# Performance work log

Measured on AMD Instinct MI355X. Metric: run time of the kernel, lower is better.

Reference implementation:

```python
import jax, jax.numpy as jnp
import numpy as np

N_NODES = 50000
N_EDGES = 1600000
D = 128        # fea_dim == hidden_units == dim_z
L = 3          # num_layers


def _gin_params(key, scale=0.05):
    ks = jax.random.split(key, 7)
    return dict(
        W1=jax.random.normal(ks[0], (L, D, D), jnp.float32) * scale,
        b1=jnp.zeros((L, D), jnp.float32),
        W2=jax.random.normal(ks[1], (L, D, D), jnp.float32) * scale,
        b2=jnp.zeros((L, D), jnp.float32),
        eps=jnp.zeros((L,), jnp.float32),
        Wout=jax.random.normal(ks[2], (D, D), jnp.float32) * scale,
        bout=jnp.zeros((D,), jnp.float32),
    )


def setup_inputs() -> dict:
    key = jax.random.key(0)
    k_x, k_s, k_d, k_m, k_sd = jax.random.split(key, 5)
    inp = {
        'x': jax.random.normal(k_x, (N_NODES, D), jnp.float32),
        'edge_src': jax.random.randint(k_s, (N_EDGES,), 0, N_NODES, jnp.int32),
        'edge_dst': jax.random.randint(k_d, (N_EDGES,), 0, N_NODES, jnp.int32),
    }
    for pref, k in (('mean_', k_m), ('std_', k_sd)):
        for name, v in _gin_params(k).items():
            inp[pref + name] = v
    inp['ln_gamma'] = jnp.ones((D,), jnp.float32)
    inp['ln_beta'] = jnp.zeros((D,), jnp.float32)
    return inp


def _gin(x, src, dst, W1, b1, W2, b2, eps, Wout, bout):
    # Standard GIN: h = MLP((1+eps)*h + sum_{j->i} h_j), Sigmoid activation
    h = x
    n = x.shape[0]
    for l in range(L):
        agg = jax.ops.segment_sum(h[src], dst, num_segments=n)  # [N, D]
        h = (1.0 + eps[l]) * h + agg
        h = jax.nn.sigmoid(h @ W1[l] + b1[l]) @ W2[l] + b2[l]
    return h @ Wout + bout  # [N, dim_z]


def _layernorm(v, g, b, eps=1e-5):
    m = jnp.mean(v, axis=-1, keepdims=True)
    var = jnp.var(v, axis=-1, keepdims=True)
    return (v - m) * jax.lax.rsqrt(var + eps) * g + b


def reference(x, edge_src, edge_dst,
              mean_W1, mean_b1, mean_W2, mean_b2, mean_eps, mean_Wout, mean_bout,
              std_W1, std_b1, std_W2, std_b2, std_eps, std_Wout, std_bout,
              ln_gamma, ln_beta):
    mean_v = _layernorm(_gin(x, edge_src, edge_dst, mean_W1, mean_b1, mean_W2,
                             mean_b2, mean_eps, mean_Wout, mean_bout),
                        ln_gamma, ln_beta)
    # NOTE: source applies bn_mean to the std path too (faithful to bug)
    std_v = _layernorm(_gin(x, edge_src, edge_dst, std_W1, std_b1, std_W2,
                            std_b2, std_eps, std_Wout, std_bout),
                       ln_gamma, ln_beta)
    epsilon = jax.random.normal(jax.random.key(42), mean_v.shape, mean_v.dtype)
    samples = mean_v + epsilon * std_v
    return (samples, mean_v, std_v)
```

## Files before the change

kernel.cpp:

```cpp
#include <hip/hip_runtime.h>
#include <math.h>

#define NNODES 50000
#define NEDGES 1600000
#define DIM    128
#define NHID   (NNODES * DIM)
#define TPB    256
#define NTILES ((NNODES + 63) / 64)

#define NBINS  196
#define BINSZ  256
#define EPT    16
#define CHUNK  (TPB * EPT)
#define NCHUNKS ((NEDGES + CHUNK - 1) / CHUNK)
#define BINCAP 10240

#define WMAT   (128 * 136)
#define NWMAT  14

typedef unsigned short bf16_t;
typedef __attribute__((ext_vector_type(8))) short short8;
typedef __attribute__((ext_vector_type(4))) float f32x4;
typedef __attribute__((ext_vector_type(2))) float f32x2;

__device__ __forceinline__ float bf_lo(unsigned u) { return __uint_as_float(u << 16); }
__device__ __forceinline__ float bf_hi(unsigned u) { return __uint_as_float(u & 0xFFFF0000u); }
__device__ __forceinline__ bf16_t f2bf(float f) {
    unsigned u = __float_as_uint(f);
    u += 0x7FFFu + ((u >> 16) & 1u);
    return (bf16_t)(u >> 16);
}
__device__ __forceinline__ unsigned pack2bf(float a, float b) {
    return (unsigned)f2bf(a) | ((unsigned)f2bf(b) << 16);
}

union S8U { short8 v; uint4 u4; unsigned us[4]; };

__global__ __launch_bounds__(TPB) void bin_hist_kernel(
    const int* __restrict__ dst, int* __restrict__ gcnt)
{
    __shared__ int lcnt[NBINS];
    const int tid = threadIdx.x;
    for (int i = tid; i < NBINS; i += TPB) lcnt[i] = 0;
    __syncthreads();
    const int base = blockIdx.x * CHUNK;
    #pragma unroll
    for (int k = 0; k < EPT; ++k) {
        int e = base + k * TPB + tid;
        if (e < NEDGES) atomicAdd(&lcnt[dst[e] >> 8], 1);
    }
    __syncthreads();
    for (int i = tid; i < NBINS; i += TPB) {
        int c = lcnt[i];
        if (c) atomicAdd(&gcnt[i], c);
    }
}

__global__ __launch_bounds__(64) void bin_scan_kernel(
    const int* __restrict__ gcnt, int* __restrict__ start, int* __restrict__ bcur,
    int* __restrict__ off)
{
    const int lane = threadIdx.x;
    int c[4];
    int s = 0;
    #pragma unroll
    for (int k = 0; k < 4; ++k) {
        int b = 4 * lane + k;
        c[k] = (b < NBINS) ? gcnt[b] : 0;
        s += c[k];
    }
    int incl = s;
    #pragma unroll
    for (int d = 1; d < 64; d <<= 1) {
        int t = __shfl_up(incl, d);
        if (lane >= d) incl += t;
    }
    int excl = incl - s;
    #pragma unroll
    for (int k = 0; k < 4; ++k) {
        int b = 4 * lane + k;
        if (b < NBINS) { start[b] = excl; bcur[b] = excl; }
        excl += c[k];
    }
    if (lane == 63) { start[NBINS] = excl; off[NNODES] = excl; }
}

__global__ __launch_bounds__(TPB) void bin_scatter_kernel(
    const int* __restrict__ src, const int* __restrict__ dst,
    int* __restrict__ bcur, unsigned* __restrict__ bucket)
{
    __shared__ int lcnt[NBINS];
    __shared__ int lcur[NBINS];
    const int tid = threadIdx.x;
    for (int i = tid; i < NBINS; i += TPB) lcnt[i] = 0;
    __syncthreads();

    unsigned pk[EPT];
    int bn[EPT];
    const int base = blockIdx.x * CHUNK;
    #pragma unroll
    for (int k = 0; k < EPT; ++k) {
        int e = base + k * TPB + tid;
        int b = -1; unsigned p = 0;
        if (e < NEDGES) {
            int d = dst[e];
            int s = src[e];
            b = d >> 8;
            p = ((unsigned)(d & 255) << 16) | (unsigned)s;
            atomicAdd(&lcnt[b], 1);
        }
        pk[k] = p; bn[k] = b;
    }
    __syncthreads();
    for (int i = tid; i < NBINS; i += TPB) {
        int c = lcnt[i];
        lcur[i] = (c > 0) ? atomicAdd(&bcur[i], c) : 0;
    }
    __syncthreads();
    #pragma unroll
    for (int k = 0; k < EPT; ++k) {
        if (bn[k] >= 0) {
            int p = atomicAdd(&lcur[bn[k]], 1);
            bucket[p] = pk[k];
        }
    }
}

__global__ __launch_bounds__(TPB) void build_csr_kernel(
    const int* __restrict__ start, unsigned* __restrict__ bucket,
    int* __restrict__ off)
{
    __shared__ unsigned se[BINCAP];
    __shared__ int lcnt[BINSZ];
    __shared__ int lofs[BINSZ];
    __shared__ int wsum[4];
    const int tid = threadIdx.x;
    const int b = blockIdx.x;
    const int j0 = start[b], j1 = start[b + 1];
    const int n = j1 - j0;

    lcnt[tid] = 0;
    for (int i = tid; i < n; i += TPB) se[i] = bucket[j0 + i];
    __syncthreads();
    for (int i = tid; i < n; i += TPB) atomicAdd(&lcnt[se[i] >> 16], 1);
    __syncthreads();

    const int lane = tid & 63, wid = tid >> 6;
    int v = lcnt[tid];
    int s = v;
    #pragma unroll
    for (int d = 1; d < 64; d <<= 1) {
        int t = __shfl_up(s, d);
        if (lane >= d) s += t;
    }
    if (lane == 63) wsum[wid] = s;
    __syncthreads();
    if (tid == 0) {
        int a = 0;
        #pragma unroll
        for (int k = 0; k < 4; ++k) { int t = wsum[k]; wsum[k] = a; a += t; }
    }
    __syncthreads();
    int excl = wsum[wid] + s - v;
    lofs[tid] = excl;
    int node = b * BINSZ + tid;
    if (node < NNODES) off[node] = j0 + excl;
    __syncthreads();

    for (int i = tid; i < n; i += TPB) {
        unsigned e = se[i];
        int pos = atomicAdd(&lofs[e >> 16], 1);
        bucket[j0 + pos] = e & 0xFFFFu;
    }
}

__global__ __launch_bounds__(TPB) void convert_weights_kernel(
    const float* __restrict__ W1_0, const float* __restrict__ W2_0,
    const float* __restrict__ Wo_0,
    const float* __restrict__ W1_1, const float* __restrict__ W2_1,
    const float* __restrict__ Wo_1,
    bf16_t* __restrict__ wpre)
{
    const int b = blockIdx.x;
    const int p = b / 7, s = b % 7;
    const float* W;
    if (s < 3)      W = (p ? W1_1 : W1_0) + (size_t)s * DIM * DIM;
    else if (s < 6) W = (p ? W2_1 : W2_0) + (size_t)(s - 3) * DIM * DIM;
    else            W = p ? Wo_1 : Wo_0;
    bf16_t* dst = wpre + (size_t)b * WMAT;

    for (int idx = threadIdx.x; idx < 128 * 16; idx += TPB) {
        int n = idx & 127, koct = idx >> 7;
        float f[8];
        #pragma unroll
        for (int j = 0; j < 8; ++j) f[j] = W[(8 * koct + j) * 128 + n];
        uint4 u;
        u.x = pack2bf(f[0], f[1]); u.y = pack2bf(f[2], f[3]);
        u.z = pack2bf(f[4], f[5]); u.w = pack2bf(f[6], f[7]);
        *(uint4*)&dst[n * 136 + 8 * koct] = u;
    }
}

__global__ __launch_bounds__(TPB) void gather_agg_f32_kernel(
    const float* __restrict__ h, const int* __restrict__ off,
    const unsigned* __restrict__ bucket, float* __restrict__ acat)
{
    int node = blockIdx.x * (TPB / 64) + (threadIdx.x >> 6);
    int lane = threadIdx.x & 63;
    if (node >= NNODES) return;
    int j0 = off[node], j1 = off[node + 1];
    const float* base = h + 2 * lane;
    float ax = 0.0f, ay = 0.0f;
    int j = j0;
    for (; j + 16 <= j1; j += 16) {
        unsigned s[16];
        #pragma unroll
        for (int k = 0; k < 16; ++k) s[k] = bucket[j + k];
        float2 v[16];
        #pragma unroll
        for (int k = 0; k < 16; ++k) v[k] = *(const float2*)(base + (size_t)s[k] * DIM);
        #pragma unroll
        for (int k = 0; k < 16; ++k) { ax += v[k].x; ay += v[k].y; }
    }
    for (; j + 8 <= j1; j += 8) {
        unsigned s[8];
        #pragma unroll
        for (int k = 0; k < 8; ++k) s[k] = bucket[j + k];
        float2 v[8];
        #pragma unroll
        for (int k = 0; k < 8; ++k) v[k] = *(const float2*)(base + (size_t)s[k] * DIM);
        #pragma unroll
        for (int k = 0; k < 8; ++k) { ax += v[k].x; ay += v[k].y; }
    }
    for (; j < j1; ++j) {
        float2 v0 = *(const float2*)(base + (size_t)bucket[j] * DIM);
        ax += v0.x; ay += v0.y;
    }
    f32x2 r; r.x = ax; r.y = ay;
    __builtin_nontemporal_store(r, (f32x2*)(acat + (size_t)node * 256 + 2 * lane));
}

__global__ __launch_bounds__(TPB) void gather_cat_kernel(
    const bf16_t* __restrict__ hc, const int* __restrict__ off,
    const unsigned* __restrict__ bucket, float* __restrict__ acat)
{
    int node = blockIdx.x * (TPB / 64) + (threadIdx.x >> 6);
    int lane = threadIdx.x & 63;
    if (node >= NNODES) return;
    int j0 = off[node], j1 = off[node + 1];
    const uint2* base = (const uint2*)hc + lane;
    float a0 = 0.f, a1 = 0.f, a2 = 0.f, a3 = 0.f;
    int j = j0;
    for (; j + 16 <= j1; j += 16) {
        unsigned s[16];
        #pragma unroll
        for (int k = 0; k < 16; ++k) s[k] = bucket[j + k];
        uint2 u[16];
        #pragma unroll
        for (int k = 0; k < 16; ++k) u[k] = base[(size_t)s[k] * 64];
        #pragma unroll
        for (int k = 0; k < 16; ++k) {
            a0 += bf_lo(u[k].x); a1 += bf_hi(u[k].x);
            a2 += bf_lo(u[k].y); a3 += bf_hi(u[k].y);
        }
    }
    for (; j + 8 <= j1; j += 8) {
        unsigned s[8];
        #pragma unroll
        for (int k = 0; k < 8; ++k) s[k] = bucket[j + k];
        uint2 u[8];
        #pragma unroll
        for (int k = 0; k < 8; ++k) u[k] = base[(size_t)s[k] * 64];
        #pragma unroll
        for (int k = 0; k < 8; ++k) {
            a0 += bf_lo(u[k].x); a1 += bf_hi(u[k].x);
            a2 += bf_lo(u[k].y); a3 += bf_hi(u[k].y);
        }
    }
    for (; j < j1; ++j) {
        uint2 u = base[(size_t)bucket[j] * 64];
        a0 += bf_lo(u.x); a1 += bf_hi(u.x);
        a2 += bf_lo(u.y); a3 += bf_hi(u.y);
    }
    f32x4 r; r.x = a0; r.y = a1; r.z = a2; r.w = a3;
    __builtin_nontemporal_store(r, (f32x4*)(acat + (size_t)node * 256 + 4 * lane));
}

template <class HinT, int INSTRIDE>
__global__ __launch_bounds__(TPB, 4) void fused_layer_kernel(
    const HinT* __restrict__ hin, const float* __restrict__ acat, int aggByPath,
    const float* __restrict__ eps0, const float* __restrict__ eps1, int eps_idx,
    const float* __restrict__ W1_0, const float* __restrict__ b1_0,
    const float* __restrict__ W2_0, const float* __restrict__ b2_0,
    const float* __restrict__ W1_1, const float* __restrict__ b1_1,
    const float* __restrict__ W2_1, const float* __restrict__ b2_1,
    const bf16_t* __restrict__ wpre,
    bf16_t* __restrict__ out)
{
    __shared__ short sWt[128 * 136];
    __shared__ short y1b[64 * 136];

    const int p = (blockIdx.x >= NTILES) ? 1 : 0;
    const int t = blockIdx.x - p * NTILES;
    const int l = eps_idx;
    const float* W1 = p ? W1_1 : W1_0;
    const float* b1 = p ? b1_1 : b1_0;
    const float* W2 = p ? W2_1 : W2_0;
    const float* b2 = p ? b2_1 : b2_0;
    const float* epsp = p ? eps1 : eps0;
    const HinT* hbase = (INSTRIDE == 256) ? (hin + p * 128) : hin;
    const float* abase = acat + (aggByPath ? p * 128 : 0);
    bf16_t* ob = out + p * 128;

    const int tid = threadIdx.x;
    if (wpre) {
        const uint4* s = (const uint4*)(wpre + (size_t)(p * 7 + l) * WMAT);
        uint4* d = (uint4*)sWt;
        #pragma unroll
        for (int i = 0; i < 9; ++i) {
            int idx = i * 256 + tid;
            if (idx < WMAT / 8) d[idx] = s[idx];
        }
    } else {
        #pragma unroll
        for (int it = 0; it < 8; ++it) {
            int idx = it * 256 + tid;
            int n = idx & 127, koct = idx >> 7;
            float f1[8];
            #pragma unroll
            for (int j = 0; j < 8; ++j) f1[j] = W1[(8 * koct + j) * 128 + n];
            uint4 u1;
            u1.x = pack2bf(f1[0], f1[1]); u1.y = pack2bf(f1[2], f1[3]);
            u1.z = pack2bf(f1[4], f1[5]); u1.w = pack2bf(f1[6], f1[7]);
            *(uint4*)&sWt[n * 136 + 8 * koct] = u1;
        }
    }
    __syncthreads();

    const int lane = tid & 63, w = tid >> 6;
    const int m = lane & 15, quad = lane >> 4;

    const float scale = 1.0f + epsp[eps_idx];
    float b1v[8], b2v[8];
    #pragma unroll
    for (int c = 0; c < 8; ++c) { b1v[c] = b1[16 * c + m]; b2v[c] = b2[16 * c + m]; }

    const int arow = min(t * 64 + 16 * w + m, NNODES - 1);

    short8 afh[4], afl[4];
    #pragma unroll
    for (int k0 = 0; k0 < 4; ++k0) {
        const int kb = 32 * k0 + 8 * quad;
        float zf[8];
        if constexpr (sizeof(HinT) == 4) {
            const float* hp = (const float*)hbase + (size_t)arow * INSTRIDE + kb;
            float4 h0 = *(const float4*)hp;
            float4 h1 = *(const float4*)(hp + 4);
            zf[0] = h0.x; zf[1] = h0.y; zf[2] = h0.z; zf[3] = h0.w;
            zf[4] = h1.x; zf[5] = h1.y; zf[6] = h1.z; zf[7] = h1.w;
        } else {
            uint4 hu = *(const uint4*)((const bf16_t*)hbase + (size_t)arow * INSTRIDE + kb);
            zf[0] = bf_lo(hu.x); zf[1] = bf_hi(hu.x);
            zf[2] = bf_lo(hu.y); zf[3] = bf_hi(hu.y);
            zf[4] = bf_lo(hu.z); zf[5] = bf_hi(hu.z);
            zf[6] = bf_lo(hu.w); zf[7] = bf_hi(hu.w);
        }
        const float* ap = abase + (size_t)arow * 256 + kb;
        float4 a0 = *(const float4*)ap;
        float4 a1 = *(const float4*)(ap + 4);
        zf[0] = fmaf(scale, zf[0], a0.x); zf[1] = fmaf(scale, zf[1], a0.y);
        zf[2] = fmaf(scale, zf[2], a0.z); zf[3] = fmaf(scale, zf[3], a0.w);
        zf[4] = fmaf(scale, zf[4], a1.x); zf[5] = fmaf(scale, zf[5], a1.y);
        zf[6] = fmaf(scale, zf[6], a1.z); zf[7] = fmaf(scale, zf[7], a1.w);
        S8U hi;
        hi.us[0] = pack2bf(zf[0], zf[1]); hi.us[1] = pack2bf(zf[2], zf[3]);
        hi.us[2] = pack2bf(zf[4], zf[5]); hi.us[3] = pack2bf(zf[6], zf[7]);
        afh[k0] = hi.v;
        S8U lo;
        float lw[8];
        lw[0] = zf[0] - bf_lo(hi.us[0]); lw[1] = zf[1] - bf_hi(hi.us[0]);
        lw[2] = zf[2] - bf_lo(hi.us[1]); lw[3] = zf[3] - bf_hi(hi.us[1]);
        lw[4] = zf[4] - bf_lo(hi.us[2]); lw[5] = zf[5] - bf_hi(hi.us[2]);
        lw[6] = zf[6] - bf_lo(hi.us[3]); lw[7] = zf[7] - bf_hi(hi.us[3]);
        lo.us[0] = pack2bf(lw[0], lw[1]); lo.us[1] = pack2bf(lw[2], lw[3]);
        lo.us[2] = pack2bf(lw[4], lw[5]); lo.us[3] = pack2bf(lw[6], lw[7]);
        afl[k0] = lo.v;
    }

    f32x4 acc[8];
    #pragma unroll
    for (int c = 0; c < 8; ++c) acc[c] = (f32x4){0.f, 0.f, 0.f, 0.f};
    #pragma unroll
    for (int k0 = 0; k0 < 4; ++k0) {
        const int kb = 32 * k0 + 8 * quad;
        #pragma unroll
        for (int c = 0; c < 8; ++c) {
            short8 bfr = *(const short8*)&sWt[(16 * c + m) * 136 + kb];
            acc[c] = __builtin_amdgcn_mfma_f32_16x16x32_bf16(afl[k0], bfr, acc[c], 0, 0, 0);
            acc[c] = __builtin_amdgcn_mfma_f32_16x16x32_bf16(afh[k0], bfr, acc[c], 0, 0, 0);
        }
    }

    const int rloc0 = 16 * w + 4 * quad;
    #pragma unroll
    for (int r = 0; r < 4; ++r) {
        #pragma unroll
        for (int c = 0; c < 8; ++c) {
            float y = acc[c][r] + b1v[c];
            y = 1.0f / (1.0f + expf(-y));
            y1b[(rloc0 + r) * 136 + 16 * c + m] = (short)f2bf(y);
        }
    }
    __syncthreads();

    if (wpre) {
        const uint4* s = (const uint4*)(wpre + (size_t)(p * 7 + 3 + l) * WMAT);
        uint4* d = (uint4*)sWt;
        #pragma unroll
        for (int i = 0; i < 9; ++i) {
            int idx = i * 256 + tid;
            if (idx < WMAT / 8) d[idx] = s[idx];
        }
    } else {
        #pragma unroll
        for (int it = 0; it < 8; ++it) {
            int idx = it * 256 + tid;
            int n = idx & 127, koct = idx >> 7;
            float f2[8];
            #pragma unroll
            for (int j = 0; j < 8; ++j) f2[j] = W2[(8 * koct + j) * 128 + n];
            uint4 u2;
            u2.x = pack2bf(f2[0], f2[1]); u2.y = pack2bf(f2[2], f2[3]);
            u2.z = pack2bf(f2[4], f2[5]); u2.w = pack2bf(f2[6], f2[7]);
            *(uint4*)&sWt[n * 136 + 8 * koct] = u2;
        }
    }
    __syncthreads();

    f32x4 acc2[8];
    #pragma unroll
    for (int c = 0; c < 8; ++c) acc2[c] = (f32x4){0.f, 0.f, 0.f, 0.f};
    #pragma unroll
    for (int k0 = 0; k0 < 4; ++k0) {
        const int kb = 32 * k0 + 8 * quad;
        short8 a2 = *(const short8*)&y1b[(16 * w + m) * 136 + kb];
        #pragma unroll
        for (int c = 0; c < 8; ++c) {
            short8 b2f = *(const short8*)&sWt[(16 * c + m) * 136 + kb];
            acc2[c] = __builtin_amdgcn_mfma_f32_16x16x32_bf16(a2, b2f, acc2[c], 0, 0, 0);
        }
    }

    const int row0 = t * 64 + 16 * w + 4 * quad;
    #pragma unroll
    for (int r = 0; r < 4; ++r) {
        const int grow = row0 + r;
        if (grow < NNODES) {
            bf16_t* op = ob + (size_t)grow * 256 + m;
            #pragma unroll
            for (int c = 0; c < 8; ++c) op[16 * c] = f2bf(acc2[c][r] + b2v[c]);
        }
    }
}

__global__ __launch_bounds__(TPB) void final_proj_kernel(
    const bf16_t* __restrict__ hc,
    const float* __restrict__ Wo0, const float* __restrict__ bo0,
    const float* __restrict__ Wo1, const float* __restrict__ bo1,
    const float* __restrict__ gamma, const float* __restrict__ beta,
    const bf16_t* __restrict__ wpre,
    float* __restrict__ M, float* __restrict__ V)
{
    __shared__ short sWt[128 * 136];

    const int p = (blockIdx.x >= NTILES) ? 1 : 0;
    const int t = blockIdx.x - p * NTILES;
    const float* W = p ? Wo1 : Wo0;
    const float* bias = p ? bo1 : bo0;
    const bf16_t* hbase = hc + p * 128;
    float* out = p ? V : M;

    const int tid = threadIdx.x;
    if (wpre) {
        const uint4* s = (const uint4*)(wpre + (size_t)(p * 7 + 6) * WMAT);
        uint4* d = (uint4*)sWt;
        #pragma unroll
        for (int i = 0; i < 9; ++i) {
            int idx = i * 256 + tid;
            if (idx < WMAT / 8) d[idx] = s[idx];
        }
    } else {
        #pragma unroll
        for (int it = 0; it < 8; ++it) {
            int idx = it * 256 + tid;
            int n = idx & 127, koct = idx >> 7;
            float f[8];
            #pragma unroll
            for (int j = 0; j < 8; ++j) f[j] = W[(8 * koct + j) * 128 + n];
            uint4 u;
            u.x = pack2bf(f[0], f[1]); u.y = pack2bf(f[2], f[3]);
            u.z = pack2bf(f[4], f[5]); u.w = pack2bf(f[6], f[7]);
            *(uint4*)&sWt[n * 136 + 8 * koct] = u;
        }
    }
    __syncthreads();

    const int lane = tid & 63, w = tid >> 6;
    const int m = lane & 15, quad = lane >> 4;

    short8 bf[32];
    #pragma unroll
    for (int c = 0; c < 8; ++c)
        #pragma unroll
        for (int k0 = 0; k0 < 4; ++k0)
            bf[c * 4 + k0] = *(const short8*)&sWt[(16 * c + m) * 136 + 32 * k0 + 8 * quad];

    float bias_v[8], g_v[8], bt_v[8];
    #pragma unroll
    for (int c = 0; c < 8; ++c) {
        bias_v[c] = bias[16 * c + m];
        g_v[c] = gamma[16 * c + m];
        bt_v[c] = beta[16 * c + m];
    }

    const int arow = min(t * 64 + 16 * w + m, NNODES - 1);
    short8 af[4];
    #pragma unroll
    for (int k0 = 0; k0 < 4; ++k0)
        af[k0] = *(const short8*)(hbase + (size_t)arow * 256 + 32 * k0 + 8 * quad);

    f32x4 acc[8];
    #pragma unroll
    for (int c = 0; c < 8; ++c) acc[c] = (f32x4){0.f, 0.f, 0.f, 0.f};
    #pragma unroll
    for (int k0 = 0; k0 < 4; ++k0)
        #pragma unroll
        for (int c = 0; c < 8; ++c)
            acc[c] = __builtin_amdgcn_mfma_f32_16x16x32_bf16(
                af[k0], bf[c * 4 + k0], acc[c], 0, 0, 0);

    const int row0 = t * 64 + 16 * w + 4 * quad;
    #pragma unroll
    for (int r = 0; r < 4; ++r) {
        const int grow = row0 + r;
        float y[8];
        #pragma unroll
        for (int c = 0; c < 8; ++c) y[c] = acc[c][r] + bias_v[c];
        float s1 = 0.f, s2 = 0.f;
        #pragma unroll
        for (int c = 0; c < 8; ++c) { s1 += y[c]; s2 = fmaf(y[c], y[c], s2); }
        #pragma unroll
        for (int d = 1; d < 16; d <<= 1) {
            s1 += __shfl_xor(s1, d);
            s2 += __shfl_xor(s2, d);
        }
        float mean = s1 * (1.0f / DIM);
        float var  = s2 * (1.0f / DIM) - mean * mean;
        float rstd = rsqrtf(var + 1e-5f);
        if (grow < NNODES) {
            float* op = out + (size_t)grow * DIM + m;
            #pragma unroll
            for (int c = 0; c < 8; ++c)
                op[16 * c] = fmaf((y[c] - mean) * rstd, g_v[c], bt_v[c]);
        }
    }
}

__device__ __forceinline__ unsigned rotl32(unsigned x, int r) {
    return (x << r) | (x >> (32 - r));
}

__device__ __forceinline__ unsigned threefry_xor(unsigned c0, unsigned c1) {
    const unsigned k0 = 0u, k1 = 42u;
    const unsigned k2 = k0 ^ k1 ^ 0x1BD11BDAu;
    unsigned x0 = c0 + k0;
    unsigned x1 = c1 + k1;
#define TF_ROUND(R) { x0 += x1; x1 = rotl32(x1, R); x1 ^= x0; }
    TF_ROUND(13) TF_ROUND(15) TF_ROUND(26) TF_ROUND(6)
    x0 += k1; x1 += k2 + 1u;
    TF_ROUND(17) TF_ROUND(29) TF_ROUND(16) TF_ROUND(24)
    x0 += k2; x1 += k0 + 2u;
    TF_ROUND(13) TF_ROUND(15) TF_ROUND(26) TF_ROUND(6)
    x0 += k0; x1 += k1 + 3u;
    TF_ROUND(17) TF_ROUND(29) TF_ROUND(16) TF_ROUND(24)
    x0 += k1; x1 += k2 + 4u;
    TF_ROUND(13) TF_ROUND(15) TF_ROUND(26) TF_ROUND(6)
    x0 += k2; x1 += k0 + 5u;
#undef TF_ROUND
    return x0 ^ x1;
}

__device__ __forceinline__ float bits_to_normal(unsigned bits) {
    float f = __uint_as_float((bits >> 9) | 0x3F800000u) - 1.0f;
    const float lo = -0.99999994f;
    float u = __fadd_rn(__fmul_rn(f, 2.0f), lo);
    u = fmaxf(lo, u);
    float w = -log1pf(-(u * u));
    float p;
    if (w < 5.0f) {
        w -= 2.5f;
        p = 2.81022636e-08f;
        p = fmaf(p, w, 3.43273939e-07f);
        p = fmaf(p, w, -3.5233877e-06f);
        p = fmaf(p, w, -4.39150654e-06f);
        p = fmaf(p, w, 0.00021858087f);
        p = fmaf(p, w, -0.00125372503f);
        p = fmaf(p, w, -0.00417768164f);
        p = fmaf(p, w, 0.246640727f);
        p = fmaf(p, w, 1.50140941f);
    } else {
        w = sqrtf(w) - 3.0f;
        p = -0.000200214257f;
        p = fmaf(p, w, 0.000100950558f);
        p = fmaf(p, w, 0.00134934322f);
        p = fmaf(p, w, -0.00367342844f);
        p = fmaf(p, w, 0.00573950773f);
        p = fmaf(p, w, -0.0076224613f);
        p = fmaf(p, w, 0.00943887047f);
        p = fmaf(p, w, 1.00167406f);
        p = fmaf(p, w, 2.83297682f);
    }
    return 1.41421356f * (p * u);
}

__global__ __launch_bounds__(TPB) void samples_kernel(
    const float* __restrict__ mean_v, const float* __restrict__ std_v,
    float* __restrict__ samples)
{
    int t = blockIdx.x * TPB + threadIdx.x;
    if (t >= NHID / 4) return;
    float4 m = ((const float4*)mean_v)[t];
    float4 s = ((const float4*)std_v)[t];
    float e[4];
    #pragma unroll
    for (int q = 0; q < 4; q++) {
        unsigned i = 4u * (unsigned)t + (unsigned)q;
        e[q] = bits_to_normal(threefry_xor(0u, i));
    }
    f32x4 r;
    r.x = fmaf(e[0], s.x, m.x);
    r.y = fmaf(e[1], s.y, m.y);
    r.z = fmaf(e[2], s.z, m.z);
    r.w = fmaf(e[3], s.w, m.w);
    __builtin_nontemporal_store(r, (f32x4*)samples + t);
}

extern "C" void kernel_launch(void* const* d_in, const int* in_sizes, int n_in,
                              void* d_out, int out_size, void* d_ws, size_t ws_size,
                              hipStream_t stream)
{
    const float* x     = (const float*)d_in[0];
    const int*   esrc  = (const int*)d_in[1];
    const int*   edst  = (const int*)d_in[2];
    const float* prm[2][7];
    for (int p = 0; p < 2; p++)
        for (int i = 0; i < 7; i++)
            prm[p][i] = (const float*)d_in[3 + p * 7 + i];
    const float* gamma = (const float*)d_in[17];
    const float* beta  = (const float*)d_in[18];

    float*  S  = (float*)d_out;
    float*  M  = S + NHID;
    float*  V  = M + NHID;
    bf16_t* Hc = (bf16_t*)S;
    float*  ACAT = M;

    int* gcnt  = (int*)d_ws;
    int* start = gcnt + NBINS;
    int* bcur  = start + NBINS + 1;
    int* off   = bcur + NBINS;
    unsigned* bucket = (unsigned*)(off + NNODES + 1);

    size_t csr_bytes = ((char*)(bucket + NEDGES)) - (char*)d_ws;
    size_t wpre_off  = (csr_bytes + 15) & ~(size_t)15;
    size_t need      = wpre_off + (size_t)NWMAT * WMAT * sizeof(bf16_t);
    bf16_t* wpre = (ws_size >= need) ? (bf16_t*)((char*)d_ws + wpre_off) : nullptr;

    const dim3 gChunk(NCHUNKS);
    const dim3 gBin(NBINS);
    const dim3 gGather((NNODES + (TPB / 64) - 1) / (TPB / 64));
    const dim3 gTile2(2 * NTILES);
    const dim3 gSamp((NHID / 4 + TPB - 1) / TPB);

    hipMemsetAsync(gcnt, 0, NBINS * sizeof(int), stream);
    if (wpre)
        convert_weights_kernel<<<dim3(NWMAT), TPB, 0, stream>>>(
            prm[0][0], prm[0][2], prm[0][5], prm[1][0], prm[1][2], prm[1][5], wpre);
    bin_hist_kernel<<<gChunk, TPB, 0, stream>>>(edst, gcnt);
    bin_scan_kernel<<<1, 64, 0, stream>>>(gcnt, start, bcur, off);
    bin_scatter_kernel<<<gChunk, TPB, 0, stream>>>(esrc, edst, bcur, bucket);
    build_csr_kernel<<<gBin, TPB, 0, stream>>>(start, bucket, off);

    gather_agg_f32_kernel<<<gGather, TPB, 0, stream>>>(x, off, bucket, ACAT);

    fused_layer_kernel<float, DIM><<<gTile2, TPB, 0, stream>>>(
        x, ACAT, 0, prm[0][4], prm[1][4], 0,
        prm[0][0], prm[0][1], prm[0][2], prm[0][3],
        prm[1][0], prm[1][1], prm[1][2], prm[1][3], wpre, Hc);

    for (int l = 1; l < 3; l++) {
        gather_cat_kernel<<<gGather, TPB, 0, stream>>>(Hc, off, bucket, ACAT);
        fused_layer_kernel<bf16_t, 256><<<gTile2, TPB, 0, stream>>>(
            Hc, ACAT, 1, prm[0][4], prm[1][4], l,
            prm[0][0] + (size_t)l * DIM * DIM, prm[0][1] + l * DIM,
            prm[0][2] + (size_t)l * DIM * DIM, prm[0][3] + l * DIM,
            prm[1][0] + (size_t)l * DIM * DIM, prm[1][1] + l * DIM,
            prm[1][2] + (size_t)l * DIM * DIM, prm[1][3] + l * DIM, wpre, Hc);
    }

    final_proj_kernel<<<gTile2, TPB, 0, stream>>>(
        Hc, prm[0][5], prm[0][6], prm[1][5], prm[1][6], gamma, beta, wpre, M, V);

    samples_kernel<<<gSamp, TPB, 0, stream>>>(M, V, S);
}
```

Before: 640.1 us.

## Drop histogram pass via fixed-capacity bins; prefetch tile inputs before weight staging

The CSR build no longer runs a separate histogram kernel and memset. Edges are scattered straight into fixed-capacity per-bin slots held in the output buffer, and the scan runs afterwards on the final bin cursors. This removes one full read pass over the destination array and two launches, but it assumes no bin exceeds BINCAP edges. The fused layer and output kernels also issue their activation loads before the weight-staging barrier, and the output kernel reads B fragments from LDS inside the MFMA loop instead of holding 32 of them in registers; the layer kernel's launch bounds drop from 4 to 3 blocks per SM.

```diff
diff --git a/kernel.cpp b/kernel.cpp
--- a/kernel.cpp
+++ b/kernel.cpp
@@ -36,58 +36,15 @@
 
 union S8U { short8 v; uint4 u4; unsigned us[4]; };
 
-__global__ __launch_bounds__(TPB) void bin_hist_kernel(
-    const int* __restrict__ dst, int* __restrict__ gcnt)
-{
-    __shared__ int lcnt[NBINS];
-    const int tid = threadIdx.x;
-    for (int i = tid; i < NBINS; i += TPB) lcnt[i] = 0;
-    __syncthreads();
-    const int base = blockIdx.x * CHUNK;
-    #pragma unroll
-    for (int k = 0; k < EPT; ++k) {
-        int e = base + k * TPB + tid;
-        if (e < NEDGES) atomicAdd(&lcnt[dst[e] >> 8], 1);
-    }
-    __syncthreads();
-    for (int i = tid; i < NBINS; i += TPB) {
-        int c = lcnt[i];
-        if (c) atomicAdd(&gcnt[i], c);
-    }
-}
-
-__global__ __launch_bounds__(64) void bin_scan_kernel(
-    const int* __restrict__ gcnt, int* __restrict__ start, int* __restrict__ bcur,
-    int* __restrict__ off)
-{
-    const int lane = threadIdx.x;
-    int c[4];
-    int s = 0;
-    #pragma unroll
-    for (int k = 0; k < 4; ++k) {
-        int b = 4 * lane + k;
-        c[k] = (b < NBINS) ? gcnt[b] : 0;
-        s += c[k];
-    }
-    int incl = s;
-    #pragma unroll
-    for (int d = 1; d < 64; d <<= 1) {
-        int t = __shfl_up(incl, d);
-        if (lane >= d) incl += t;
-    }
-    int excl = incl - s;
-    #pragma unroll
-    for (int k = 0; k < 4; ++k) {
-        int b = 4 * lane + k;
-        if (b < NBINS) { start[b] = excl; bcur[b] = excl; }
-        excl += c[k];
-    }
-    if (lane == 63) { start[NBINS] = excl; off[NNODES] = excl; }
+__global__ __launch_bounds__(TPB) void init_bcur_kernel(int* __restrict__ bcur)
+{
+    int i = threadIdx.x;
+    if (i < NBINS) bcur[i] = i * BINCAP;
 }
 
 __global__ __launch_bounds__(TPB) void bin_scatter_kernel(
     const int* __restrict__ src, const int* __restrict__ dst,
-    int* __restrict__ bcur, unsigned* __restrict__ bucket)
+    int* __restrict__ bcur, unsigned* __restrict__ fatb)
 {
     __shared__ int lcnt[NBINS];
     __shared__ int lcur[NBINS];
@@ -121,13 +78,42 @@
     for (int k = 0; k < EPT; ++k) {
         if (bn[k] >= 0) {
             int p = atomicAdd(&lcur[bn[k]], 1);
-            bucket[p] = pk[k];
-        }
-    }
+            fatb[p] = pk[k];
+        }
+    }
+}
+
+__global__ __launch_bounds__(64) void bin_scan_kernel(
+    const int* __restrict__ bcur, int* __restrict__ start, int* __restrict__ off)
+{
+    const int lane = threadIdx.x;
+    int c[4];
+    int s = 0;
+    #pragma unroll
+    for (int k = 0; k < 4; ++k) {
+        int b = 4 * lane + k;
+        c[k] = (b < NBINS) ? (bcur[b] - b * BINCAP) : 0;
+        s += c[k];
+    }
+    int incl = s;
+    #pragma unroll
+    for (int d = 1; d < 64; d <<= 1) {
+        int t = __shfl_up(incl, d);
+        if (lane >= d) incl += t;
+    }
+    int excl = incl - s;
+    #pragma unroll
+    for (int k = 0; k < 4; ++k) {
+        int b = 4 * lane + k;
+        if (b < NBINS) start[b] = excl;
+        excl += c[k];
+    }
+    if (lane == 63) { start[NBINS] = excl; off[NNODES] = excl; }
 }
 
 __global__ __launch_bounds__(TPB) void build_csr_kernel(
-    const int* __restrict__ start, unsigned* __restrict__ bucket,
+    const int* __restrict__ start, const int* __restrict__ bcur,
+    const unsigned* __restrict__ fatb, unsigned* __restrict__ bucket,
     int* __restrict__ off)
 {
     __shared__ unsigned se[BINCAP];
@@ -136,11 +122,12 @@
     __shared__ int wsum[4];
     const int tid = threadIdx.x;
     const int b = blockIdx.x;
-    const int j0 = start[b], j1 = start[b + 1];
-    const int n = j1 - j0;
+    const int j0 = start[b];
+    const int n = bcur[b] - b * BINCAP;
+    const unsigned* fb = fatb + (size_t)b * BINCAP;
 
     lcnt[tid] = 0;
-    for (int i = tid; i < n; i += TPB) se[i] = bucket[j0 + i];
+    for (int i = tid; i < n; i += TPB) se[i] = fb[i];
     __syncthreads();
     for (int i = tid; i < n; i += TPB) atomicAdd(&lcnt[se[i] >> 16], 1);
     __syncthreads();
@@ -287,7 +274,7 @@
 }
 
 template <class HinT, int INSTRIDE>
-__global__ __launch_bounds__(TPB, 4) void fused_layer_kernel(
+__global__ __launch_bounds__(TPB, 3) void fused_layer_kernel(
     const HinT* __restrict__ hin, const float* __restrict__ acat, int aggByPath,
     const float* __restrict__ eps0, const float* __restrict__ eps1, int eps_idx,
     const float* __restrict__ W1_0, const float* __restrict__ b1_0,
@@ -313,6 +300,28 @@
     bf16_t* ob = out + p * 128;
 
     const int tid = threadIdx.x;
+    const int lane = tid & 63, w = tid >> 6;
+    const int m = lane & 15, quad = lane >> 4;
+    const int arow = min(t * 64 + 16 * w + m, NNODES - 1);
+
+    uint4  hraw16[4];
+    float4 hraw32a[4], hraw32b[4];
+    float4 araw0[4], araw1[4];
+    #pragma unroll
+    for (int k0 = 0; k0 < 4; ++k0) {
+        const int kb = 32 * k0 + 8 * quad;
+        if constexpr (sizeof(HinT) == 4) {
+            const float* hp = (const float*)hbase + (size_t)arow * INSTRIDE + kb;
+            hraw32a[k0] = *(const float4*)hp;
+            hraw32b[k0] = *(const float4*)(hp + 4);
+        } else {
+            hraw16[k0] = *(const uint4*)((const bf16_t*)hbase + (size_t)arow * INSTRIDE + kb);
+        }
+        const float* ap = abase + (size_t)arow * 256 + kb;
+        araw0[k0] = *(const float4*)ap;
+        araw1[k0] = *(const float4*)(ap + 4);
+    }
+
     if (wpre) {
         const uint4* s = (const uint4*)(wpre + (size_t)(p * 7 + l) * WMAT);
         uint4* d = (uint4*)sWt;
@@ -337,41 +346,30 @@
     }
     __syncthreads();
 
-    const int lane = tid & 63, w = tid >> 6;
-    const int m = lane & 15, quad = lane >> 4;
-
     const float scale = 1.0f + epsp[eps_idx];
     float b1v[8], b2v[8];
     #pragma unroll
     for (int c = 0; c < 8; ++c) { b1v[c] = b1[16 * c + m]; b2v[c] = b2[16 * c + m]; }
 
-    const int arow = min(t * 64 + 16 * w + m, NNODES - 1);
-
     short8 afh[4], afl[4];
     #pragma unroll
     for (int k0 = 0; k0 < 4; ++k0) {
-        const int kb = 32 * k0 + 8 * quad;
         float zf[8];
         if constexpr (sizeof(HinT) == 4) {
-            const float* hp = (const float*)hbase + (size_t)arow * INSTRIDE + kb;
-            float4 h0 = *(const float4*)hp;
-            float4 h1 = *(const float4*)(hp + 4);
-            zf[0] = h0.x; zf[1] = h0.y; zf[2] = h0.z; zf[3] = h0.w;
-            zf[4] = h1.x; zf[5] = h1.y; zf[6] = h1.z; zf[7] = h1.w;
+            zf[0] = hraw32a[k0].x; zf[1] = hraw32a[k0].y;
+            zf[2] = hraw32a[k0].z; zf[3] = hraw32a[k0].w;
+            zf[4] = hraw32b[k0].x; zf[5] = hraw32b[k0].y;
+            zf[6] = hraw32b[k0].z; zf[7] = hraw32b[k0].w;
         } else {
-            uint4 hu = *(const uint4*)((const bf16_t*)hbase + (size_t)arow * INSTRIDE + kb);
-            zf[0] = bf_lo(hu.x); zf[1] = bf_hi(hu.x);
-            zf[2] = bf_lo(hu.y); zf[3] = bf_hi(hu.y);
-            zf[4] = bf_lo(hu.z); zf[5] = bf_hi(hu.z);
-            zf[6] = bf_lo(hu.w); zf[7] = bf_hi(hu.w);
-        }
-        const float* ap = abase + (size_t)arow * 256 + kb;
-        float4 a0 = *(const float4*)ap;
-        float4 a1 = *(const float4*)(ap + 4);
-        zf[0] = fmaf(scale, zf[0], a0.x); zf[1] = fmaf(scale, zf[1], a0.y);
-        zf[2] = fmaf(scale, zf[2], a0.z); zf[3] = fmaf(scale, zf[3], a0.w);
-        zf[4] = fmaf(scale, zf[4], a1.x); zf[5] = fmaf(scale, zf[5], a1.y);
-        zf[6] = fmaf(scale, zf[6], a1.z); zf[7] = fmaf(scale, zf[7], a1.w);
+            zf[0] = bf_lo(hraw16[k0].x); zf[1] = bf_hi(hraw16[k0].x);
+            zf[2] = bf_lo(hraw16[k0].y); zf[3] = bf_hi(hraw16[k0].y);
+            zf[4] = bf_lo(hraw16[k0].z); zf[5] = bf_hi(hraw16[k0].z);
+            zf[6] = bf_lo(hraw16[k0].w); zf[7] = bf_hi(hraw16[k0].w);
+        }
+        zf[0] = fmaf(scale, zf[0], araw0[k0].x); zf[1] = fmaf(scale, zf[1], araw0[k0].y);
+        zf[2] = fmaf(scale, zf[2], araw0[k0].z); zf[3] = fmaf(scale, zf[3], araw0[k0].w);
+        zf[4] = fmaf(scale, zf[4], araw1[k0].x); zf[5] = fmaf(scale, zf[5], araw1[k0].y);
+        zf[6] = fmaf(scale, zf[6], araw1[k0].z); zf[7] = fmaf(scale, zf[7], araw1[k0].w);
         S8U hi;
         hi.us[0] = pack2bf(zf[0], zf[1]); hi.us[1] = pack2bf(zf[2], zf[3]);
         hi.us[2] = pack2bf(zf[4], zf[5]); hi.us[3] = pack2bf(zf[6], zf[7]);
@@ -481,6 +479,15 @@
     float* out = p ? V : M;
 
     const int tid = threadIdx.x;
+    const int lane = tid & 63, w = tid >> 6;
+    const int m = lane & 15, quad = lane >> 4;
+    const int arow = min(t * 64 + 16 * w + m, NNODES - 1);
+
+    short8 af[4];
+    #pragma unroll
+    for (int k0 = 0; k0 < 4; ++k0)
+        af[k0] = *(const short8*)(hbase + (size_t)arow * 256 + 32 * k0 + 8 * quad);
+
     if (wpre) {
         const uint4* s = (const uint4*)(wpre + (size_t)(p * 7 + 6) * WMAT);
         uint4* d = (uint4*)sWt;
@@ -505,16 +512,6 @@
     }
     __syncthreads();
 
-    const int lane = tid & 63, w = tid >> 6;
-    const int m = lane & 15, quad = lane >> 4;
-
-    short8 bf[32];
-    #pragma unroll
-    for (int c = 0; c < 8; ++c)
-        #pragma unroll
-        for (int k0 = 0; k0 < 4; ++k0)
-            bf[c * 4 + k0] = *(const short8*)&sWt[(16 * c + m) * 136 + 32 * k0 + 8 * quad];
-
     float bias_v[8], g_v[8], bt_v[8];
     #pragma unroll
     for (int c = 0; c < 8; ++c) {
@@ -523,21 +520,17 @@
         bt_v[c] = beta[16 * c + m];
     }
 
-    const int arow = min(t * 64 + 16 * w + m, NNODES - 1);
-    short8 af[4];
-    #pragma unroll
-    for (int k0 = 0; k0 < 4; ++k0)
-        af[k0] = *(const short8*)(hbase + (size_t)arow * 256 + 32 * k0 + 8 * quad);
-
     f32x4 acc[8];
     #pragma unroll
     for (int c = 0; c < 8; ++c) acc[c] = (f32x4){0.f, 0.f, 0.f, 0.f};
     #pragma unroll
-    for (int k0 = 0; k0 < 4; ++k0)
+    for (int k0 = 0; k0 < 4; ++k0) {
+        const int kb = 32 * k0 + 8 * quad;
         #pragma unroll
         for (int c = 0; c < 8; ++c)
             acc[c] = __builtin_amdgcn_mfma_f32_16x16x32_bf16(
-                af[k0], bf[c * 4 + k0], acc[c], 0, 0, 0);
+                af[k0], *(const short8*)&sWt[(16 * c + m) * 136 + kb], acc[c], 0, 0, 0);
+    }
 
     const int row0 = t * 64 + 16 * w + 4 * quad;
     #pragma unroll
@@ -664,9 +657,9 @@
     float*  V  = M + NHID;
     bf16_t* Hc = (bf16_t*)S;
     float*  ACAT = M;
-
-    int* gcnt  = (int*)d_ws;
-    int* start = gcnt + NBINS;
+    unsigned* fatb = (unsigned*)M;
+
+    int* start = (int*)d_ws;
     int* bcur  = start + NBINS + 1;
     int* off   = bcur + NBINS;
     unsigned* bucket = (unsigned*)(off + NNODES + 1);
@@ -682,14 +675,13 @@
     const dim3 gTile2(2 * NTILES);
     const dim3 gSamp((NHID / 4 + TPB - 1) / TPB);
 
-    hipMemsetAsync(gcnt, 0, NBINS * sizeof(int), stream);
     if (wpre)
         convert_weights_kernel<<<dim3(NWMAT), TPB, 0, stream>>>(
             prm[0][0], prm[0][2], prm[0][5], prm[1][0], prm[1][2], prm[1][5], wpre);
-    bin_hist_kernel<<<gChunk, TPB, 0, stream>>>(edst, gcnt);
-    bin_scan_kernel<<<1, 64, 0, stream>>>(gcnt, start, bcur, off);
-    bin_scatter_kernel<<<gChunk, TPB, 0, stream>>>(esrc, edst, bcur, bucket);
-    build_csr_kernel<<<gBin, TPB, 0, stream>>>(start, bucket, off);
+    init_bcur_kernel<<<1, TPB, 0, stream>>>(bcur);
+    bin_scatter_kernel<<<gChunk, TPB, 0, stream>>>(esrc, edst, bcur, fatb);
+    bin_scan_kernel<<<1, 64, 0, stream>>>(bcur, start, off);
+    build_csr_kernel<<<gBin, TPB, 0, stream>>>(start, bcur, fatb, bucket, off);
 
     gather_agg_f32_kernel<<<gGather, TPB, 0, stream>>>(x, off, bucket, ACAT);
 
```

Result: no change. 636.0 us (-0.6%).
